# Kernel optimization log

Hardware: AMD Instinct MI355X
Metric: run time of the kernel (lower is better)

The kernel has to match this reference:

```python
import jax, jax.numpy as jnp
import numpy as np

N, F_IN, F_OUT, C = 4096, 512, 256, 4


def setup_inputs() -> dict:
    key = jax.random.key(0)
    k1, k2, k3, k4 = jax.random.split(key, 4)
    stdv = 1.0 / np.sqrt(F_OUT)
    x = jax.random.normal(k1, (N, F_IN), dtype=jnp.float32)
    adjs = jax.random.normal(k2, (N, N, C), dtype=jnp.float32)
    weight = jax.random.uniform(k3, (F_IN, F_OUT, C), dtype=jnp.float32, minval=-stdv, maxval=stdv)
    bias = jax.random.uniform(k4, (N, F_OUT, C), dtype=jnp.float32, minval=-stdv, maxval=stdv)
    return {"x": x, "adjs": adjs, "weight": weight, "bias": bias}


def _fft_product(X, Y):
    # t-product: FFT along channel axis, per-frequency matmul, IFFT, real part
    Xf = jnp.fft.fft(X, axis=-1)
    Yf = jnp.fft.fft(Y, axis=-1)
    Zf = jnp.einsum('ijk,jrk->irk', Xf, Yf)
    return jnp.fft.ifft(Zf, axis=-1).real.astype(X.dtype)


def reference(x, adjs, weight, bias):
    C_ = adjs.shape[-1]
    # x.repeat(C,1,1).permute(1,2,0) -> [N, F, C]
    x3 = jnp.broadcast_to(x[:, :, None], (x.shape[0], x.shape[1], C_))
    h = _fft_product(x3, weight)      # [N, F_OUT, C]
    out = _fft_product(adjs, h)       # [N, F_OUT, C]
    return out + bias
```

## Files before the change

### kernel.cpp

```cpp
#include <hip/hip_runtime.h>
#include <cstdint>
#include <cstddef>

#define NN   4096
#define FIN  512
#define FOUT 256

typedef short bf16x8 __attribute__((ext_vector_type(8)));
typedef float f32x4  __attribute__((ext_vector_type(4)));
typedef float f32x2  __attribute__((ext_vector_type(2)));

__device__ __forceinline__ unsigned short f2bf(float f) {
    union { float f; unsigned u; } v; v.f = f;
    unsigned r = v.u + 0x7FFFu + ((v.u >> 16) & 1u);
    return (unsigned short)(r >> 16);
}
__device__ __forceinline__ unsigned pack2(float a, float b) {
    return (unsigned)f2bf(a) | ((unsigned)f2bf(b) << 16);
}

__global__ __launch_bounds__(256) void k_prep_wsum(const f32x4* __restrict__ w4,
                                                   unsigned short* __restrict__ wsumT) {
    int t = blockIdx.x * 256 + threadIdx.x;
    int r = t & (FOUT - 1);
    int j = t >> 8;
    f32x4 v = w4[j * FOUT + r];
    wsumT[r * FIN + j] = f2bf((v.x + v.y) + (v.z + v.w));
}

__global__ __launch_bounds__(512) void k_gemm_h(const float* __restrict__ x,
                                                const unsigned short* __restrict__ Bt,
                                                unsigned short* __restrict__ Ht) {
    __shared__ unsigned short Abf[16 * 72];
    const int tid  = threadIdx.x;
    const int lane = tid & 63;
    const int wave = tid >> 6;
    const int quad = lane >> 4;
    const int l15  = lane & 15;
    const int i0   = blockIdx.x * 16;
    const int si   = tid >> 5;
    const int sk   = (tid & 31) * 2;

    f32x4 acc0 = {0.f, 0.f, 0.f, 0.f};
    f32x4 acc1 = {0.f, 0.f, 0.f, 0.f};

    f32x2 pf;
    bf16x8 bp00, bp01, bp10, bp11;

    auto loadA = [&](int c) {
        pf = *(const f32x2*)(x + (size_t)(i0 + si) * FIN + c * 64 + sk);
    };
    auto loadB = [&](int c, bf16x8& b00, bf16x8& b01, bf16x8& b10, bf16x8& b11) {
        const unsigned short* p0 = Bt + (size_t)(wave * 32 + l15) * FIN + c * 64 + quad * 8;
        b00 = *(const bf16x8*)(p0);
        b01 = *(const bf16x8*)(p0 + 32);
        const unsigned short* p1 = p0 + (size_t)16 * FIN;
        b10 = *(const bf16x8*)(p1);
        b11 = *(const bf16x8*)(p1 + 32);
    };

    loadA(0);
    loadB(0, bp00, bp01, bp10, bp11);

    for (int c = 0; c < FIN / 64; ++c) {
        __syncthreads();
        *(unsigned*)&Abf[si * 72 + sk] = pack2(pf.x, pf.y);
        __syncthreads();

        bf16x8 bc00 = bp00, bc01 = bp01, bc10 = bp10, bc11 = bp11;
        if (c + 1 < FIN / 64) {
            loadA(c + 1);
            loadB(c + 1, bp00, bp01, bp10, bp11);
        }
        bf16x8 a0 = *(const bf16x8*)&Abf[l15 * 72 + quad * 8];
        bf16x8 a1 = *(const bf16x8*)&Abf[l15 * 72 + 32 + quad * 8];

        acc0 = __builtin_amdgcn_mfma_f32_16x16x32_bf16(a0, bc00, acc0, 0, 0, 0);
        acc0 = __builtin_amdgcn_mfma_f32_16x16x32_bf16(a1, bc01, acc0, 0, 0, 0);
        acc1 = __builtin_amdgcn_mfma_f32_16x16x32_bf16(a0, bc10, acc1, 0, 0, 0);
        acc1 = __builtin_amdgcn_mfma_f32_16x16x32_bf16(a1, bc11, acc1, 0, 0, 0);
    }

    const int n  = wave * 32 + l15;
    const int ib = i0 + quad * 4;
    ushort4 h;
    h.x = f2bf(acc0[0]); h.y = f2bf(acc0[1]); h.z = f2bf(acc0[2]); h.w = f2bf(acc0[3]);
    *(ushort4*)(Ht + (size_t)n * NN + ib) = h;
    h.x = f2bf(acc1[0]); h.y = f2bf(acc1[1]); h.z = f2bf(acc1[2]); h.w = f2bf(acc1[3]);
    *(ushort4*)(Ht + (size_t)(n + 16) * NN + ib) = h;
}

#define LD 72
__global__ __launch_bounds__(512) void k_gemm_big(const f32x4* __restrict__ adjs4,
                                                  const unsigned short* __restrict__ Bt,
                                                  float* __restrict__ P) {
    __shared__ unsigned short Abf[2][64 * LD];

    const int tid  = threadIdx.x;
    const int lane = tid & 63;
    const int wave = tid >> 6;
    const int quad = lane >> 4;
    const int l15  = lane & 15;

    const int kq   = blockIdx.x & 3;
    const int rg   = blockIdx.x >> 2;
    const int row0 = rg * 64;
    const size_t kbase = (size_t)kq * 1024;

    const int sr = tid >> 3;
    const int sc = tid & 7;

    f32x4 acc[4][2];
#pragma unroll
    for (int m = 0; m < 4; ++m)
#pragma unroll
        for (int n = 0; n < 2; ++n)
            acc[m][n] = (f32x4){0.f, 0.f, 0.f, 0.f};

    f32x4 pa[8];
    bf16x8 pb[2][2];

    auto loadA = [&](int c) {
        const f32x4* ap = adjs4 + (size_t)(row0 + sr) * NN + kbase + c * 64;
#pragma unroll
        for (int u = 0; u < 4; ++u) {
            pa[2 * u]     = __builtin_nontemporal_load(ap + sc * 2 + u * 16);
            pa[2 * u + 1] = __builtin_nontemporal_load(ap + sc * 2 + u * 16 + 1);
        }
    };
    auto writeA = [&](int b) {
        unsigned* dst = (unsigned*)&Abf[b][sr * LD + sc * 2];
#pragma unroll
        for (int u = 0; u < 4; ++u) {
            f32x4 p0 = pa[2 * u], p1 = pa[2 * u + 1];
            dst[u * 8] = pack2((p0.x + p0.y) + (p0.z + p0.w),
                               (p1.x + p1.y) + (p1.z + p1.w));
        }
    };
    auto loadB = [&](int c) {
#pragma unroll
        for (int n = 0; n < 2; ++n) {
            const unsigned short* p = Bt + (size_t)(wave * 32 + n * 16 + l15) * NN
                                        + kbase + c * 64 + quad * 8;
            pb[n][0] = *(const bf16x8*)p;
            pb[n][1] = *(const bf16x8*)(p + 32);
        }
    };

    loadA(0);
    loadB(0);

    for (int c = 0; c < 16; ++c) {
        const int b = c & 1;
        writeA(b);
        if (c + 1 < 16) loadA(c + 1);
        __syncthreads();

        bf16x8 bc[2][2] = {{pb[0][0], pb[0][1]}, {pb[1][0], pb[1][1]}};
        if (c + 1 < 16) loadB(c + 1);

#pragma unroll
        for (int s = 0; s < 2; ++s) {
#pragma unroll
            for (int m = 0; m < 4; ++m) {
                bf16x8 a = *(const bf16x8*)&Abf[b][(m * 16 + l15) * LD + s * 32 + quad * 8];
                acc[m][0] = __builtin_amdgcn_mfma_f32_16x16x32_bf16(a, bc[0][s], acc[m][0], 0, 0, 0);
                acc[m][1] = __builtin_amdgcn_mfma_f32_16x16x32_bf16(a, bc[1][s], acc[m][1], 0, 0, 0);
            }
        }
        __syncthreads();
    }

    float* p = P + (size_t)kq * NN * FOUT;
#pragma unroll
    for (int m = 0; m < 4; ++m) {
#pragma unroll
        for (int n = 0; n < 2; ++n) {
            const int col = wave * 32 + n * 16 + l15;
#pragma unroll
            for (int r = 0; r < 4; ++r) {
                const int row = row0 + m * 16 + quad * 4 + r;
                p[(size_t)row * FOUT + col] = acc[m][n][r];
            }
        }
    }
}

__global__ __launch_bounds__(256) void k_reduce(const float* __restrict__ P,
                                                const f32x4* __restrict__ bias4,
                                                f32x4* __restrict__ out4) {
    const int idx = blockIdx.x * 256 + threadIdx.x;
    const size_t STR = (size_t)NN * FOUT;
    float s = (P[idx] + P[idx + STR]) + (P[idx + 2 * STR] + P[idx + 3 * STR]);
    f32x4 bv = bias4[idx];
    f32x4 o;
    o.x = s + bv.x; o.y = s + bv.y; o.z = s + bv.z; o.w = s + bv.w;
    out4[idx] = o;
}

extern "C" void kernel_launch(void* const* d_in, const int* in_sizes, int n_in,
                              void* d_out, int out_size, void* d_ws, size_t ws_size,
                              hipStream_t stream) {
    const float* x     = (const float*)d_in[0];
    const f32x4* adjs4 = (const f32x4*)d_in[1];
    const f32x4* w4    = (const f32x4*)d_in[2];
    const f32x4* bias4 = (const f32x4*)d_in[3];
    f32x4*       out4  = (f32x4*)d_out;

    char* ws = (char*)d_ws;
    unsigned short* wsumT = (unsigned short*)ws;
    unsigned short* Ht    = (unsigned short*)(ws + 262144);
    float*          Pp    = (float*)(ws + 262144 + 2097152);

    k_prep_wsum<<<(FIN * FOUT) / 256, 256, 0, stream>>>(w4, wsumT);
    k_gemm_h<<<NN / 16, 512, 0, stream>>>(x, wsumT, Ht);
    k_gemm_big<<<256, 512, 0, stream>>>(adjs4, Ht, Pp);
    k_reduce<<<(NN * FOUT) / 256, 256, 0, stream>>>(Pp, bias4, out4);
}
```

Baseline: 396.9 us.

## Retile big GEMM to 32-row blocks with 128-wide K steps and a doubled grid

The adjacency GEMM kernel now uses 32-row tiles with a 128-wide K chunk and launches twice as many blocks, 512 instead of 256, so more of the GPU's compute units have work. It also adds an occupancy hint to the launch bounds and drops the trailing per-iteration barrier, which the double buffer makes safe. The adjacency loads change from nontemporal to plain loads, and the partial-sum stores become nontemporal. The B operand is no longer prefetched one step ahead but loaded in the same iteration, which may expose global load latency. Halving the rows per block also halves reuse of each loaded B tile.

After: 433.3 us. 9.2% more time.

```diff
diff --git a/kernel.cpp b/kernel.cpp
--- a/kernel.cpp
+++ b/kernel.cpp
@@ -90,11 +90,12 @@
     *(ushort4*)(Ht + (size_t)(n + 16) * NN + ib) = h;
 }
 
-#define LD 72
-__global__ __launch_bounds__(512) void k_gemm_big(const f32x4* __restrict__ adjs4,
-                                                  const unsigned short* __restrict__ Bt,
-                                                  float* __restrict__ P) {
-    __shared__ unsigned short Abf[2][64 * LD];
+#define BIGBK 128
+#define LDB   136
+__global__ __launch_bounds__(512, 4) void k_gemm_big(const f32x4* __restrict__ adjs4,
+                                                     const unsigned short* __restrict__ Bt,
+                                                     float* __restrict__ P) {
+    __shared__ __align__(16) unsigned short Abf[2][32 * LDB];
 
     const int tid  = threadIdx.x;
     const int lane = tid & 63;
@@ -104,83 +105,78 @@
 
     const int kq   = blockIdx.x & 3;
     const int rg   = blockIdx.x >> 2;
-    const int row0 = rg * 64;
+    const int row0 = rg * 32;
     const size_t kbase = (size_t)kq * 1024;
 
-    const int sr = tid >> 3;
-    const int sc = tid & 7;
-
-    f32x4 acc[4][2];
-#pragma unroll
-    for (int m = 0; m < 4; ++m)
+    const int sr = tid >> 4;
+    const int sc = tid & 15;
+
+    f32x4 acc[2][2];
+#pragma unroll
+    for (int m = 0; m < 2; ++m)
 #pragma unroll
         for (int n = 0; n < 2; ++n)
             acc[m][n] = (f32x4){0.f, 0.f, 0.f, 0.f};
 
     f32x4 pa[8];
-    bf16x8 pb[2][2];
 
     auto loadA = [&](int c) {
-        const f32x4* ap = adjs4 + (size_t)(row0 + sr) * NN + kbase + c * 64;
+        const f32x4* ap = adjs4 + (size_t)(row0 + sr) * NN + kbase + c * BIGBK + sc * 2;
 #pragma unroll
         for (int u = 0; u < 4; ++u) {
-            pa[2 * u]     = __builtin_nontemporal_load(ap + sc * 2 + u * 16);
-            pa[2 * u + 1] = __builtin_nontemporal_load(ap + sc * 2 + u * 16 + 1);
+            pa[2 * u]     = ap[u * 32];
+            pa[2 * u + 1] = ap[u * 32 + 1];
         }
     };
     auto writeA = [&](int b) {
-        unsigned* dst = (unsigned*)&Abf[b][sr * LD + sc * 2];
+        unsigned* dst = (unsigned*)&Abf[b][sr * LDB];
 #pragma unroll
         for (int u = 0; u < 4; ++u) {
             f32x4 p0 = pa[2 * u], p1 = pa[2 * u + 1];
-            dst[u * 8] = pack2((p0.x + p0.y) + (p0.z + p0.w),
-                               (p1.x + p1.y) + (p1.z + p1.w));
-        }
-    };
-    auto loadB = [&](int c) {
+            dst[sc + u * 16] = pack2((p0.x + p0.y) + (p0.z + p0.w),
+                                     (p1.x + p1.y) + (p1.z + p1.w));
+        }
+    };
+
+    loadA(0);
+
+    for (int c = 0; c < 8; ++c) {
+        const int b = c & 1;
+        writeA(b);
+        if (c + 1 < 8) loadA(c + 1);
+        __syncthreads();
+
+        bf16x8 pb[2][4];
 #pragma unroll
         for (int n = 0; n < 2; ++n) {
             const unsigned short* p = Bt + (size_t)(wave * 32 + n * 16 + l15) * NN
-                                        + kbase + c * 64 + quad * 8;
-            pb[n][0] = *(const bf16x8*)p;
-            pb[n][1] = *(const bf16x8*)(p + 32);
-        }
-    };
-
-    loadA(0);
-    loadB(0);
-
-    for (int c = 0; c < 16; ++c) {
-        const int b = c & 1;
-        writeA(b);
-        if (c + 1 < 16) loadA(c + 1);
-        __syncthreads();
-
-        bf16x8 bc[2][2] = {{pb[0][0], pb[0][1]}, {pb[1][0], pb[1][1]}};
-        if (c + 1 < 16) loadB(c + 1);
-
-#pragma unroll
-        for (int s = 0; s < 2; ++s) {
-#pragma unroll
-            for (int m = 0; m < 4; ++m) {
-                bf16x8 a = *(const bf16x8*)&Abf[b][(m * 16 + l15) * LD + s * 32 + quad * 8];
-                acc[m][0] = __builtin_amdgcn_mfma_f32_16x16x32_bf16(a, bc[0][s], acc[m][0], 0, 0, 0);
-                acc[m][1] = __builtin_amdgcn_mfma_f32_16x16x32_bf16(a, bc[1][s], acc[m][1], 0, 0, 0);
+                                        + kbase + c * BIGBK + quad * 8;
+#pragma unroll
+            for (int s = 0; s < 4; ++s)
+                pb[n][s] = *(const bf16x8*)(p + s * 32);
+        }
+
+#pragma unroll
+        for (int s = 0; s < 4; ++s) {
+#pragma unroll
+            for (int m = 0; m < 2; ++m) {
+                bf16x8 a = *(const bf16x8*)&Abf[b][(m * 16 + l15) * LDB + s * 32 + quad * 8];
+                acc[m][0] = __builtin_amdgcn_mfma_f32_16x16x32_bf16(a, pb[0][s], acc[m][0], 0, 0, 0);
+                acc[m][1] = __builtin_amdgcn_mfma_f32_16x16x32_bf16(a, pb[1][s], acc[m][1], 0, 0, 0);
             }
         }
-        __syncthreads();
     }
 
     float* p = P + (size_t)kq * NN * FOUT;
 #pragma unroll
-    for (int m = 0; m < 4; ++m) {
+    for (int m = 0; m < 2; ++m) {
 #pragma unroll
         for (int n = 0; n < 2; ++n) {
             const int col = wave * 32 + n * 16 + l15;
 #pragma unroll
             for (int r = 0; r < 4; ++r) {
                 const int row = row0 + m * 16 + quad * 4 + r;
-                p[(size_t)row * FOUT + col] = acc[m][n][r];
+                __builtin_nontemporal_store(acc[m][n][r], &p[(size_t)row * FOUT + col]);
             }
         }
     }
@@ -214,6 +210,6 @@
 
     k_prep_wsum<<<(FIN * FOUT) / 256, 256, 0, stream>>>(w4, wsumT);
     k_gemm_h<<<NN / 16, 512, 0, stream>>>(x, wsumT, Ht);
-    k_gemm_big<<<256, 512, 0, stream>>>(adjs4, Ht, Pp);
+    k_gemm_big<<<512, 512, 0, stream>>>(adjs4, Ht, Pp);
     k_reduce<<<(NN * FOUT) / 256, 256, 0, stream>>>(Pp, bias4, out4);
 }
```
